# Optimization experiments

Measured on AMD Instinct MI355X. Metric: run time of the kernel, lower is better.

The kernel has to match this reference:

```python
import jax, jax.numpy as jnp
import numpy as np

N_QUBITS = 5
N_A = 1
N_LAYERS = 4
PATCH = 2 ** (N_QUBITS - N_A)  # 16

CNOT4 = jnp.array([[1, 0, 0, 0], [0, 1, 0, 0], [0, 0, 0, 1], [0, 0, 1, 0]], dtype=jnp.complex64)


def _ry(t):
    c = jnp.cos(t / 2).astype(jnp.complex64)
    s = jnp.sin(t / 2).astype(jnp.complex64)
    return jnp.stack([jnp.stack([c, -s]), jnp.stack([s, c])])


def _rot(phi, theta, omega):
    # PennyLane Rot = RZ(omega) RY(theta) RZ(phi)
    c = jnp.cos(theta / 2)
    s = jnp.sin(theta / 2)
    ep = jnp.exp(-0.5j * (phi + omega))  # e^{-i(phi+omega)/2}
    em = jnp.exp(-0.5j * (phi - omega))  # e^{-i(phi-omega)/2}
    return jnp.stack([jnp.stack([ep * c, -jnp.conj(em) * s]),
                      jnp.stack([em * s, jnp.conj(ep) * c])])


def _apply_1q(state, U, w):
    # contract U onto qubit axis w of state [2]*5
    s = jnp.tensordot(U, state, axes=(1, w))
    return jnp.moveaxis(s, 0, w)


def _apply_cnot(state, c, t):
    perm = jnp.moveaxis(state, (c, t), (0, 1))
    shp = perm.shape
    out = (CNOT4 @ perm.reshape(4, -1)).reshape(shp)
    return jnp.moveaxis(out, (0, 1), (c, t))


def _simulate(noise, w):
    # noise: [5], w: [4,5,3] -> normalized probs over first 16 basis states
    state = jnp.zeros((2,) * N_QUBITS, jnp.complex64).at[(0,) * N_QUBITS].set(1.0)
    for q in range(N_QUBITS):
        state = _apply_1q(state, _ry(noise[q]), q)
    for l in range(N_LAYERS):
        r = l % (N_QUBITS - 1) + 1  # StronglyEntanglingLayers default ranges
        for q in range(N_QUBITS):
            state = _apply_1q(state, _rot(w[l, q, 0], w[l, q, 1], w[l, q, 2]), q)
        for q in range(N_QUBITS):
            state = _apply_cnot(state, q, (q + r) % N_QUBITS)
    probs = jnp.abs(state.reshape(-1)) ** 2  # [32]
    p0 = probs[:PATCH] / jnp.sum(probs)  # partial measure: ancilla wire 4 == 0
    return p0 / jnp.max(p0)


def setup_inputs() -> dict:
    key = jax.random.key(0)
    k1, k2 = jax.random.split(key)
    B, G = 65536, 4
    x = jax.random.uniform(k1, (B, N_QUBITS), dtype=jnp.float32)
    weights = jax.random.uniform(k2, (G, N_LAYERS, N_QUBITS, 3), dtype=jnp.float32)  # q_delta=1
    return {"x": x, "weights": weights}


def reference(x, weights):
    sim_g = jax.vmap(_simulate, in_axes=(None, 0))   # over generators
    sim_bg = jax.vmap(sim_g, in_axes=(0, None))      # over batch
    out = sim_bg(x, weights)                         # [B, G, 16]
    return out.reshape(x.shape[0], -1).astype(jnp.float32)  # [B, G*16]
```

## Files before the change

### kernel.cpp

```cpp
#include <hip/hip_runtime.h>


#define NGEN 4
#define NLAY 4
#define NQ   5

typedef _Float16 half8 __attribute__((ext_vector_type(8)));
typedef float    f32x4 __attribute__((ext_vector_type(4)));

__global__ __launch_bounds__(256) void pqg_fused(
    const float* __restrict__ x,
    const float* __restrict__ wts,
    float* __restrict__ out)
{
    __shared__ float gm[NLAY * NQ * 8];
    __shared__ float Mr[16 * 33];
    __shared__ float Mi[16 * 33];
    __shared__ __align__(16) _Float16 afr[512];
    __shared__ __align__(16) _Float16 afi[512];
    __shared__ float scC[512 * 5];
    __shared__ float scS[512 * 5];

    const int t  = threadIdx.x;
    const int g  = blockIdx.x & 3;
    const int b0 = (blockIdx.x >> 2) * 512;

    {
        const float2* xb = (const float2*)(x + (size_t)b0 * 5);
#pragma unroll
        for (int i = 0; i < 5; ++i) {
            const int e = i * 256 + t;
            const float2 v = xb[e];
            scS[2 * e + 0] = __sinf(0.5f * v.x);
            scC[2 * e + 0] = __cosf(0.5f * v.x);
            scS[2 * e + 1] = __sinf(0.5f * v.y);
            scC[2 * e + 1] = __cosf(0.5f * v.y);
        }
    }

    if (t < NLAY * NQ) {
        const float* wp = wts + (g * (NLAY * NQ) + t) * 3;
        const float phi = wp[0], theta = wp[1], omega = wp[2];
        const float a = 0.5f * (phi + omega);
        const float bb = 0.5f * (phi - omega);
        const float h = 0.5f * theta;
        const float sa = __sinf(a), ca = __cosf(a);
        const float sb = __sinf(bb), cb = __cosf(bb);
        const float st = __sinf(h), ct = __cosf(h);
        float* m = &gm[t * 8];
        m[0] =  ca * ct;  m[1] = -sa * ct;
        m[2] = -cb * st;  m[3] = -sb * st;
        m[4] =  cb * st;  m[5] = -sb * st;
        m[6] =  ca * ct;  m[7] =  sa * ct;
    }

#pragma unroll
    for (int h = 0; h < 2; ++h) {
        const int idx = h * 256 + t;
        const int r = idx >> 5, c = idx & 31;
        Mr[r * 33 + c] = (r == c) ? 1.0f : 0.0f;
        Mi[r * 33 + c] = 0.0f;
    }
    __syncthreads();

    const int row = t & 15;
    const int p   = t >> 4;

#pragma clang loop unroll(disable)
    for (int l = NLAY - 1; l >= 0; --l) {
        {
            const int c0 = p, c1 = p + 16;
            int v0 = c0, v1 = c1;
#pragma unroll
            for (int q = 0; q < NQ; ++q) {
                const int cb = 16 >> q;
                int tq = q + l + 1; if (tq >= NQ) tq -= NQ;
                const int tb = 16 >> tq;
                if (v0 & cb) v0 ^= tb;
                if (v1 & cb) v1 ^= tb;
            }
            const float a0r = Mr[row * 33 + v0], a0i = Mi[row * 33 + v0];
            const float a1r = Mr[row * 33 + v1], a1i = Mi[row * 33 + v1];
            __syncthreads();
            Mr[row * 33 + c0] = a0r;  Mi[row * 33 + c0] = a0i;
            Mr[row * 33 + c1] = a1r;  Mi[row * 33 + c1] = a1i;
            __syncthreads();
        }
#pragma clang loop unroll(disable)
        for (int q = NQ - 1; q >= 0; --q) {
            const float* m = &gm[(l * NQ + q) * 8];
            const float u00r = m[0], u00i = m[1], u01r = m[2], u01i = m[3];
            const float u10r = m[4], u10i = m[5], u11r = m[6], u11i = m[7];
            const int sb = 16 >> q;
            const int lowm = sb - 1;
            const int i = ((p & ~lowm) << 1) | (p & lowm);
            const int j = i | sb;
            const int ii = row * 33 + i, jj = row * 33 + j;
            const float ar = Mr[ii], ai = Mi[ii];
            const float br = Mr[jj], bi = Mi[jj];
            Mr[ii] = u00r * ar - u00i * ai + u10r * br - u10i * bi;
            Mi[ii] = u00r * ai + u00i * ar + u10r * bi + u10i * br;
            Mr[jj] = u01r * ar - u01i * ai + u11r * br - u11i * bi;
            Mi[jj] = u01r * ai + u01i * ar + u11r * bi + u11i * br;
            __syncthreads();
        }
    }

#pragma unroll
    for (int h = 0; h < 2; ++h) {
        const int idx = h * 256 + t;
        const int k = idx >> 4, m = idx & 15;
        const int L = (k >> 3) * 16 + m;
        const int jj = k & 7;
        afr[L * 8 + jj] = (_Float16)Mr[m * 33 + k];
        afi[L * 8 + jj] = (_Float16)Mi[m * 33 + k];
    }
    __syncthreads();

    const int lane = t & 63;
    const int wv   = t >> 6;
    const int quad = lane >> 4;
    const int n    = lane & 15;

    const half8 Ar = *(const half8*)&afr[lane * 8];
    const half8 Ai = *(const half8*)&afi[lane * 8];

#pragma unroll
    for (int t8 = 0; t8 < 8; ++t8) {
        const int bl = wv * 128 + t8 * 16 + n;
        const int b  = b0 + bl;
        const float* C = &scC[bl * 5];
        const float* S = &scS[bl * 5];

        const float f01 = ((quad & 2) ? S[0] : C[0]) * ((quad & 1) ? S[1] : C[1]);
        const float a0 = f01 * C[2], a1 = f01 * S[2];
        const float b00 = a0 * C[3], b01 = a0 * S[3];
        const float b10 = a1 * C[3], b11 = a1 * S[3];

        half8 Bf;
        Bf[0] = (_Float16)(b00 * C[4]);  Bf[1] = (_Float16)(b00 * S[4]);
        Bf[2] = (_Float16)(b01 * C[4]);  Bf[3] = (_Float16)(b01 * S[4]);
        Bf[4] = (_Float16)(b10 * C[4]);  Bf[5] = (_Float16)(b10 * S[4]);
        Bf[6] = (_Float16)(b11 * C[4]);  Bf[7] = (_Float16)(b11 * S[4]);

        f32x4 accR = {0.f, 0.f, 0.f, 0.f};
        f32x4 accI = {0.f, 0.f, 0.f, 0.f};
        accR = __builtin_amdgcn_mfma_f32_16x16x32_f16(Ar, Bf, accR, 0, 0, 0);
        accI = __builtin_amdgcn_mfma_f32_16x16x32_f16(Ai, Bf, accI, 0, 0, 0);

        const float p0 = accR[0] * accR[0] + accI[0] * accI[0];
        const float p1 = accR[1] * accR[1] + accI[1] * accI[1];
        const float p2 = accR[2] * accR[2] + accI[2] * accI[2];
        const float p3 = accR[3] * accR[3] + accI[3] * accI[3];

        float mx = fmaxf(fmaxf(p0, p1), fmaxf(p2, p3));
        mx = fmaxf(mx, __shfl_xor(mx, 16));
        mx = fmaxf(mx, __shfl_xor(mx, 32));
        const float inv = 1.0f / mx;

        const float4 o = make_float4(p0 * inv, p1 * inv, p2 * inv, p3 * inv);
        *(float4*)(out + (size_t)b * 64 + g * 16 + quad * 4) = o;
    }
}

extern "C" void kernel_launch(void* const* d_in, const int* in_sizes, int n_in,
                              void* d_out, int out_size, void* d_ws, size_t ws_size,
                              hipStream_t stream) {
    const float* x = (const float*)d_in[0];
    const float* w = (const float*)d_in[1];
    float* out = (float*)d_out;
    const int B = in_sizes[0] / NQ;

    pqg_fused<<<(B / 512) * NGEN, 256, 0, stream>>>(x, w, out);
}
```

Before: 68.28 us.

## Split unitary construction into a separate kernel and batch all generators per block

Moves the per-generator circuit-unitary construction into a small prologue kernel that writes fp16 MFMA operands to workspace. The main kernel then loads all four generator matrices and handles every generator for 128 batch rows per block. This removes the redundant, sync-heavy matrix build that each block previously repeated, and makes the output writes cover contiguous full rows. It adds a second launch and a dependency on workspace memory.

```diff
diff --git a/kernel.cpp b/kernel.cpp
--- a/kernel.cpp
+++ b/kernel.cpp
@@ -8,35 +8,16 @@
 typedef _Float16 half8 __attribute__((ext_vector_type(8)));
 typedef float    f32x4 __attribute__((ext_vector_type(4)));
 
-__global__ __launch_bounds__(256) void pqg_fused(
-    const float* __restrict__ x,
+__global__ __launch_bounds__(256) void pqg_build(
     const float* __restrict__ wts,
-    float* __restrict__ out)
+    _Float16* __restrict__ ws)
 {
     __shared__ float gm[NLAY * NQ * 8];
     __shared__ float Mr[16 * 33];
     __shared__ float Mi[16 * 33];
-    __shared__ __align__(16) _Float16 afr[512];
-    __shared__ __align__(16) _Float16 afi[512];
-    __shared__ float scC[512 * 5];
-    __shared__ float scS[512 * 5];
 
-    const int t  = threadIdx.x;
-    const int g  = blockIdx.x & 3;
-    const int b0 = (blockIdx.x >> 2) * 512;
-
-    {
-        const float2* xb = (const float2*)(x + (size_t)b0 * 5);
-#pragma unroll
-        for (int i = 0; i < 5; ++i) {
-            const int e = i * 256 + t;
-            const float2 v = xb[e];
-            scS[2 * e + 0] = __sinf(0.5f * v.x);
-            scC[2 * e + 0] = __cosf(0.5f * v.x);
-            scS[2 * e + 1] = __sinf(0.5f * v.y);
-            scC[2 * e + 1] = __cosf(0.5f * v.y);
-        }
-    }
+    const int t = threadIdx.x;
+    const int g = blockIdx.x;
 
     if (t < NLAY * NQ) {
         const float* wp = wts + (g * (NLAY * NQ) + t) * 3;
@@ -112,22 +93,48 @@
         const int k = idx >> 4, m = idx & 15;
         const int L = (k >> 3) * 16 + m;
         const int jj = k & 7;
-        afr[L * 8 + jj] = (_Float16)Mr[m * 33 + k];
-        afi[L * 8 + jj] = (_Float16)Mi[m * 33 + k];
+        ws[g * 1024 + L * 8 + jj]       = (_Float16)Mr[m * 33 + k];
+        ws[g * 1024 + 512 + L * 8 + jj] = (_Float16)Mi[m * 33 + k];
     }
-    __syncthreads();
+}
+
+#define BPB 128
+
+__global__ __launch_bounds__(256) void pqg_gemm(
+    const float* __restrict__ x,
+    const _Float16* __restrict__ wsH,
+    float* __restrict__ out)
+{
+    __shared__ float scC[BPB * 5];
+    __shared__ float scS[BPB * 5];
+
+    const int t  = threadIdx.x;
+    const int b0 = blockIdx.x * BPB;
+
+    if (t < 160) {
+        const float4 v = ((const float4*)(x + (size_t)b0 * 5))[t];
+        scS[4 * t + 0] = __sinf(0.5f * v.x);  scC[4 * t + 0] = __cosf(0.5f * v.x);
+        scS[4 * t + 1] = __sinf(0.5f * v.y);  scC[4 * t + 1] = __cosf(0.5f * v.y);
+        scS[4 * t + 2] = __sinf(0.5f * v.z);  scC[4 * t + 2] = __cosf(0.5f * v.z);
+        scS[4 * t + 3] = __sinf(0.5f * v.w);  scC[4 * t + 3] = __cosf(0.5f * v.w);
+    }
 
     const int lane = t & 63;
     const int wv   = t >> 6;
     const int quad = lane >> 4;
     const int n    = lane & 15;
 
-    const half8 Ar = *(const half8*)&afr[lane * 8];
-    const half8 Ai = *(const half8*)&afi[lane * 8];
+    half8 Ar[NGEN], Ai[NGEN];
+#pragma unroll
+    for (int g = 0; g < NGEN; ++g) {
+        Ar[g] = *(const half8*)&wsH[g * 1024 + lane * 8];
+        Ai[g] = *(const half8*)&wsH[g * 1024 + 512 + lane * 8];
+    }
+    __syncthreads();
 
 #pragma unroll
-    for (int t8 = 0; t8 < 8; ++t8) {
-        const int bl = wv * 128 + t8 * 16 + n;
+    for (int tt = 0; tt < 2; ++tt) {
+        const int bl = wv * 32 + tt * 16 + n;
         const int b  = b0 + bl;
         const float* C = &scC[bl * 5];
         const float* S = &scS[bl * 5];
@@ -143,23 +150,26 @@
         Bf[4] = (_Float16)(b10 * C[4]);  Bf[5] = (_Float16)(b10 * S[4]);
         Bf[6] = (_Float16)(b11 * C[4]);  Bf[7] = (_Float16)(b11 * S[4]);
 
-        f32x4 accR = {0.f, 0.f, 0.f, 0.f};
-        f32x4 accI = {0.f, 0.f, 0.f, 0.f};
-        accR = __builtin_amdgcn_mfma_f32_16x16x32_f16(Ar, Bf, accR, 0, 0, 0);
-        accI = __builtin_amdgcn_mfma_f32_16x16x32_f16(Ai, Bf, accI, 0, 0, 0);
+#pragma unroll
+        for (int g = 0; g < NGEN; ++g) {
+            f32x4 accR = {0.f, 0.f, 0.f, 0.f};
+            f32x4 accI = {0.f, 0.f, 0.f, 0.f};
+            accR = __builtin_amdgcn_mfma_f32_16x16x32_f16(Ar[g], Bf, accR, 0, 0, 0);
+            accI = __builtin_amdgcn_mfma_f32_16x16x32_f16(Ai[g], Bf, accI, 0, 0, 0);
 
-        const float p0 = accR[0] * accR[0] + accI[0] * accI[0];
-        const float p1 = accR[1] * accR[1] + accI[1] * accI[1];
-        const float p2 = accR[2] * accR[2] + accI[2] * accI[2];
-        const float p3 = accR[3] * accR[3] + accI[3] * accI[3];
+            const float p0 = accR[0] * accR[0] + accI[0] * accI[0];
+            const float p1 = accR[1] * accR[1] + accI[1] * accI[1];
+            const float p2 = accR[2] * accR[2] + accI[2] * accI[2];
+            const float p3 = accR[3] * accR[3] + accI[3] * accI[3];
 
-        float mx = fmaxf(fmaxf(p0, p1), fmaxf(p2, p3));
-        mx = fmaxf(mx, __shfl_xor(mx, 16));
-        mx = fmaxf(mx, __shfl_xor(mx, 32));
-        const float inv = 1.0f / mx;
+            float mx = fmaxf(fmaxf(p0, p1), fmaxf(p2, p3));
+            mx = fmaxf(mx, __shfl_xor(mx, 16));
+            mx = fmaxf(mx, __shfl_xor(mx, 32));
+            const float inv = 1.0f / mx;
 
-        const float4 o = make_float4(p0 * inv, p1 * inv, p2 * inv, p3 * inv);
-        *(float4*)(out + (size_t)b * 64 + g * 16 + quad * 4) = o;
+            const float4 o = make_float4(p0 * inv, p1 * inv, p2 * inv, p3 * inv);
+            *(float4*)(out + (size_t)b * 64 + g * 16 + quad * 4) = o;
+        }
     }
 }
 
@@ -169,7 +179,9 @@
     const float* x = (const float*)d_in[0];
     const float* w = (const float*)d_in[1];
     float* out = (float*)d_out;
+    _Float16* ws = (_Float16*)d_ws;
     const int B = in_sizes[0] / NQ;
 
-    pqg_fused<<<(B / 512) * NGEN, 256, 0, stream>>>(x, w, out);
+    pqg_build<<<NGEN, 256, 0, stream>>>(w, ws);
+    pqg_gemm<<<B / BPB, 256, 0, stream>>>(x, ws, out);
 }
```

After: 68.72 us. No clear change (+0.7%).
